# Kernel optimization log

Hardware: AMD Instinct MI355X
Metric: run time of the kernel (lower is better)

The kernel has to match this reference:

```python
import jax, jax.numpy as jnp
import numpy as np

QMAX = 127.0  # int8 symmetric range


def _fake_quant(x, axes):
    """AQT-style int8 symmetric fake-quant over contraction axes.

    Returns quantized integer values (stored as f32) and per-channel scales
    (keepdims over `axes`).
    """
    absmax = jnp.max(jnp.abs(x), axis=axes, keepdims=True)
    scale = jnp.where(absmax > 0, absmax / QMAX, jnp.ones_like(absmax))
    q = jnp.clip(jnp.round(x / scale), -QMAX, QMAX)
    return q, scale


def setup_inputs() -> dict:
    key = jax.random.key(0)
    k1, k2 = jax.random.split(key)
    lhs = jax.random.normal(k1, (4, 16384, 512), dtype=jnp.float32)
    rhs = jax.random.normal(k2, (512, 512), dtype=jnp.float32)
    return {"lhs": lhs, "rhs": rhs}


def reference(lhs, rhs):
    # dimension_numbers = (((2,), (0,)), ((), ())) -- Dense-style contraction.
    # Quantize each operand symmetrically to int8 along its contraction axis.
    lhs_q, lhs_scale = _fake_quant(lhs, axes=(2,))   # lhs_q: [B,S,D], scale: [B,S,1]
    rhs_q, rhs_scale = _fake_quant(rhs, axes=(0,))   # rhs_q: [D,F], scale: [1,F]
    # Integer-valued matmul (accumulation exact in f32 for these magnitudes),
    # then dequantize with the outer product of scales.
    acc = jnp.einsum('bsd,df->bsf', lhs_q, rhs_q)    # [B,S,F]
    return acc * lhs_scale * rhs_scale               # broadcast [B,S,1]*[1,F]
```

## Files before the change

kernel.cpp:

```cpp
#include <hip/hip_runtime.h>
#include <hip/hip_bf16.h>
#include <stdint.h>

#define QMAX 127.0f

typedef __attribute__((ext_vector_type(4))) int   i32x4;
typedef __attribute__((ext_vector_type(2))) int   i32x2;
typedef __attribute__((ext_vector_type(4))) float f32x4v;

typedef __attribute__((address_space(1))) const void GVoid;
typedef __attribute__((address_space(3))) void LVoid;

__device__ inline int quant_i(float x, float inv) {
    float q = rintf(x * inv);
    q = fminf(fmaxf(q, -QMAX), QMAX);
    return (int)q;
}

__device__ inline uint32_t pack4(f32x4v v, float inv) {
    return (uint32_t)(quant_i(v.x, inv) & 255)
         | ((uint32_t)(quant_i(v.y, inv) & 255) << 8)
         | ((uint32_t)(quant_i(v.z, inv) & 255) << 16)
         | ((uint32_t)(quant_i(v.w, inv) & 255) << 24);
}

__device__ inline float amax8(f32x4v a, f32x4v b) {
    return fmaxf(fmaxf(fmaxf(fabsf(a.x), fabsf(a.y)), fmaxf(fabsf(a.z), fabsf(a.w))),
                 fmaxf(fmaxf(fabsf(b.x), fabsf(b.y)), fmaxf(fabsf(b.z), fabsf(b.w))));
}

__global__ __launch_bounds__(256, 8) void quant_kernel(const float* __restrict__ lhs,
                                                       const float* __restrict__ rhs,
                                                       int8_t* __restrict__ Aq,
                                                       int8_t* __restrict__ Bt,
                                                       float* __restrict__ lscale,
                                                       float* __restrict__ rscale,
                                                       int nLhs) {
    const int lane = threadIdx.x & 63;
    const int wave = threadIdx.x >> 6;
    const int bid  = blockIdx.x;

    if (bid >= nLhs) {
        const int f = (bid - nLhs) * 4 + wave;
        float v[8];
        float amax = 0.f;
#pragma unroll
        for (int i = 0; i < 8; ++i) {
            v[i] = rhs[(size_t)(lane + 64 * i) * 512 + f];
            amax = fmaxf(amax, fabsf(v[i]));
        }
#pragma unroll
        for (int m = 1; m <= 32; m <<= 1)
            amax = fmaxf(amax, __shfl_xor(amax, m, 64));
        const float inv = amax > 0.f ? QMAX / amax : 0.f;
        if (lane == 0) rscale[f] = amax > 0.f ? amax * (1.0f / QMAX) : 1.0f;
#pragma unroll
        for (int i = 0; i < 8; ++i)
            Bt[(size_t)f * 512 + lane + 64 * i] = (int8_t)quant_i(v[i], inv);
        return;
    }

    const int row0 = bid * 32 + wave * 8;
    const float* rp = lhs + (size_t)row0 * 512 + lane * 8;
    int8_t* op = Aq + (size_t)row0 * 512 + lane * 8;
#pragma unroll
    for (int r = 0; r < 8; r += 2) {
        const f32x4v a0 = __builtin_nontemporal_load((const f32x4v*)(rp + (size_t)r * 512));
        const f32x4v b0 = __builtin_nontemporal_load((const f32x4v*)(rp + (size_t)r * 512 + 4));
        const f32x4v a1 = __builtin_nontemporal_load((const f32x4v*)(rp + (size_t)(r + 1) * 512));
        const f32x4v b1 = __builtin_nontemporal_load((const f32x4v*)(rp + (size_t)(r + 1) * 512 + 4));
        float m0 = amax8(a0, b0);
        float m1 = amax8(a1, b1);
#pragma unroll
        for (int m = 1; m <= 32; m <<= 1) {
            m0 = fmaxf(m0, __shfl_xor(m0, m, 64));
            m1 = fmaxf(m1, __shfl_xor(m1, m, 64));
        }
        const float inv0 = m0 > 0.f ? QMAX / m0 : 0.f;
        const float inv1 = m1 > 0.f ? QMAX / m1 : 0.f;
        if (lane == 0) {
            lscale[row0 + r]     = m0 > 0.f ? m0 * (1.0f / QMAX) : 1.0f;
            lscale[row0 + r + 1] = m1 > 0.f ? m1 * (1.0f / QMAX) : 1.0f;
        }
        i32x2 p0, p1;
        p0.x = (int)pack4(a0, inv0); p0.y = (int)pack4(b0, inv0);
        p1.x = (int)pack4(a1, inv1); p1.y = (int)pack4(b1, inv1);
        *(i32x2*)(op + (size_t)r * 512)       = p0;
        *(i32x2*)(op + (size_t)(r + 1) * 512) = p1;
    }
}

__global__ __launch_bounds__(256, 2) void gemm_kernel(const int8_t* __restrict__ Aq,
                                                      const int8_t* __restrict__ Bt,
                                                      const float* __restrict__ lscale,
                                                      const float* __restrict__ rscale,
                                                      float* __restrict__ out) {
    __shared__ int8_t lds[65536];

    const int tid  = threadIdx.x;
    const int lane = tid & 63;
    const int wave = tid >> 6;
    const int wr   = wave >> 1;
    const int wc   = wave & 1;

    const int g   = blockIdx.x;
    const int xcd = g & 7;
    const int j   = g >> 3;
    const int m0  = (xcd * 64 + (j >> 2)) * 128;
    const int n0  = (j & 3) * 128;

    const int lane15 = lane & 15;
    const int laneHi = lane >> 4;
    const int chunkBase = wave * 1024;

    i32x4 acc[4][4];
#pragma unroll
    for (int i = 0; i < 4; ++i)
#pragma unroll
        for (int jj = 0; jj < 4; ++jj)
            acc[i][jj] = (i32x4){0, 0, 0, 0};

#define STAGE(KT, BUF)                                                              \
    {                                                                               \
        _Pragma("unroll")                                                           \
        for (int c = 0; c < 4; ++c) {                                               \
            const int chunk = c * 4096 + chunkBase;                                 \
            const int d     = chunk + lane * 16;                                    \
            const int row   = d >> 7;                                               \
            const int srck  = (d & 127) ^ ((row & 7) << 4);                         \
            const int8_t* sA = Aq + (size_t)(m0 + row) * 512 + (KT) + srck;         \
            __builtin_amdgcn_global_load_lds((GVoid*)sA, (LVoid*)(lds + (BUF) + chunk), 16, 0, 0); \
            const int8_t* sB = Bt + (size_t)(n0 + row) * 512 + (KT) + srck;         \
            __builtin_amdgcn_global_load_lds((GVoid*)sB, (LVoid*)(lds + (BUF) + 16384 + chunk), 16, 0, 0); \
        }                                                                           \
    }

    STAGE(0, 0)
    __syncthreads();

#pragma unroll
    for (int t = 0; t < 4; ++t) {
        const int buf = (t & 1) * 32768;
        if (t < 3) STAGE((t + 1) * 128, (~t & 1) * 32768)

        i32x4 af[4][2], bf[4][2];
#pragma unroll
        for (int mi = 0; mi < 4; ++mi) {
            const int row = wr * 64 + mi * 16 + lane15;
            const int sw  = (row & 7) << 4;
#pragma unroll
            for (int kk = 0; kk < 2; ++kk) {
                const int kb = kk * 64 + laneHi * 16;
                af[mi][kk] = *(const i32x4*)(lds + buf + row * 128 + (kb ^ sw));
            }
        }
#pragma unroll
        for (int ni = 0; ni < 4; ++ni) {
            const int col = wc * 64 + ni * 16 + lane15;
            const int sw  = (col & 7) << 4;
#pragma unroll
            for (int kk = 0; kk < 2; ++kk) {
                const int kb = kk * 64 + laneHi * 16;
                bf[ni][kk] = *(const i32x4*)(lds + buf + 16384 + col * 128 + (kb ^ sw));
            }
        }
#pragma unroll
        for (int kk = 0; kk < 2; ++kk)
#pragma unroll
            for (int mi = 0; mi < 4; ++mi)
#pragma unroll
                for (int ni = 0; ni < 4; ++ni)
                    acc[mi][ni] = __builtin_amdgcn_mfma_i32_16x16x64_i8(
                        af[mi][kk], bf[ni][kk], acc[mi][ni], 0, 0, 0);

        if (t < 3) __syncthreads();
    }
#undef STAGE

    float rs[4];
#pragma unroll
    for (int ni = 0; ni < 4; ++ni)
        rs[ni] = rscale[n0 + wc * 64 + ni * 16 + lane15];
    const int rg = laneHi * 4;
#pragma unroll
    for (int mi = 0; mi < 4; ++mi) {
#pragma unroll
        for (int r = 0; r < 4; ++r) {
            const int grow = m0 + wr * 64 + mi * 16 + rg + r;
            const float ls = lscale[grow];
            float* op = out + (size_t)grow * 512 + n0 + wc * 64;
#pragma unroll
            for (int ni = 0; ni < 4; ++ni)
                __builtin_nontemporal_store(acc[mi][ni][r] * ls * rs[ni],
                                            op + ni * 16 + lane15);
        }
    }
}

extern "C" void kernel_launch(void* const* d_in, const int* in_sizes, int n_in,
                              void* d_out, int out_size, void* d_ws, size_t ws_size,
                              hipStream_t stream) {
    const float* lhs = (const float*)d_in[0];
    const float* rhs = (const float*)d_in[1];
    float* out = (float*)d_out;

    char* ws = (char*)d_ws;
    int8_t* Bt    = (int8_t*)ws;
    float* rscale = (float*)(ws + 262144);
    float* lscale = (float*)(ws + 266240);
    int8_t* Aq    = (int8_t*)(ws + 1048576);

    const int rows = in_sizes[0] / 512;
    const int nLhs = rows / 32;

    quant_kernel<<<nLhs + 128, 256, 0, stream>>>(lhs, rhs, Aq, Bt, lscale, rscale, nLhs);
    gemm_kernel<<<(rows / 128) * 4, 256, 0, stream>>>(Aq, Bt, lscale, rscale, out);
}
```

Baseline: 77.31 us.

## Drop GEMM LDS double buffering to single buffer for higher occupancy

The GEMM kernel now uses one 32 KB LDS buffer instead of a 64 KB double buffer. It raises the launch-bounds occupancy hint from 2 to 3 blocks per CU, so more blocks can hide load latency. Each k-tile now loads, syncs, computes and syncs again, which gives up the overlap of prefetching the next tile with MFMA work. The output stores also change from nontemporal to plain stores.

```diff
diff --git a/kernel.cpp b/kernel.cpp
--- a/kernel.cpp
+++ b/kernel.cpp
@@ -90,12 +90,12 @@
     }
 }
 
-__global__ __launch_bounds__(256, 2) void gemm_kernel(const int8_t* __restrict__ Aq,
+__global__ __launch_bounds__(256, 3) void gemm_kernel(const int8_t* __restrict__ Aq,
                                                       const int8_t* __restrict__ Bt,
                                                       const float* __restrict__ lscale,
                                                       const float* __restrict__ rscale,
                                                       float* __restrict__ out) {
-    __shared__ int8_t lds[65536];
+    __shared__ int8_t lds[32768];
 
     const int tid  = threadIdx.x;
     const int lane = tid & 63;
@@ -109,39 +109,32 @@
     const int m0  = (xcd * 64 + (j >> 2)) * 128;
     const int n0  = (j & 3) * 128;
 
+    i32x4 acc[4][4];
+#pragma unroll
+    for (int i = 0; i < 4; ++i)
+#pragma unroll
+        for (int jj = 0; jj < 4; ++jj)
+            acc[i][jj] = (i32x4){0, 0, 0, 0};
+
     const int lane15 = lane & 15;
     const int laneHi = lane >> 4;
-    const int chunkBase = wave * 1024;
-
-    i32x4 acc[4][4];
-#pragma unroll
-    for (int i = 0; i < 4; ++i)
-#pragma unroll
-        for (int jj = 0; jj < 4; ++jj)
-            acc[i][jj] = (i32x4){0, 0, 0, 0};
-
-#define STAGE(KT, BUF)                                                              \
-    {                                                                               \
-        _Pragma("unroll")                                                           \
-        for (int c = 0; c < 4; ++c) {                                               \
-            const int chunk = c * 4096 + chunkBase;                                 \
-            const int d     = chunk + lane * 16;                                    \
-            const int row   = d >> 7;                                               \
-            const int srck  = (d & 127) ^ ((row & 7) << 4);                         \
-            const int8_t* sA = Aq + (size_t)(m0 + row) * 512 + (KT) + srck;         \
-            __builtin_amdgcn_global_load_lds((GVoid*)sA, (LVoid*)(lds + (BUF) + chunk), 16, 0, 0); \
-            const int8_t* sB = Bt + (size_t)(n0 + row) * 512 + (KT) + srck;         \
-            __builtin_amdgcn_global_load_lds((GVoid*)sB, (LVoid*)(lds + (BUF) + 16384 + chunk), 16, 0, 0); \
-        }                                                                           \
-    }
-
-    STAGE(0, 0)
-    __syncthreads();
-
-#pragma unroll
-    for (int t = 0; t < 4; ++t) {
-        const int buf = (t & 1) * 32768;
-        if (t < 3) STAGE((t + 1) * 128, (~t & 1) * 32768)
+
+#pragma unroll
+    for (int kt = 0; kt < 512; kt += 128) {
+        __syncthreads();
+#pragma unroll
+        for (int c = 0; c < 4; ++c) {
+            const int chunk = (c * 4 + wave) * 1024;
+            const int d     = chunk + lane * 16;
+            const int row   = d >> 7;
+            const int koff  = d & 127;
+            const int srck  = koff ^ ((row & 7) << 4);
+            const int8_t* srcA = Aq + (size_t)(m0 + row) * 512 + kt + srck;
+            __builtin_amdgcn_global_load_lds((GVoid*)srcA, (LVoid*)(lds + chunk), 16, 0, 0);
+            const int8_t* srcB = Bt + (size_t)(n0 + row) * 512 + kt + srck;
+            __builtin_amdgcn_global_load_lds((GVoid*)srcB, (LVoid*)(lds + 16384 + chunk), 16, 0, 0);
+        }
+        __syncthreads();
 
         i32x4 af[4][2], bf[4][2];
 #pragma unroll
@@ -151,7 +144,7 @@
 #pragma unroll
             for (int kk = 0; kk < 2; ++kk) {
                 const int kb = kk * 64 + laneHi * 16;
-                af[mi][kk] = *(const i32x4*)(lds + buf + row * 128 + (kb ^ sw));
+                af[mi][kk] = *(const i32x4*)(lds + row * 128 + (kb ^ sw));
             }
         }
 #pragma unroll
@@ -161,7 +154,7 @@
 #pragma unroll
             for (int kk = 0; kk < 2; ++kk) {
                 const int kb = kk * 64 + laneHi * 16;
-                bf[ni][kk] = *(const i32x4*)(lds + buf + 16384 + col * 128 + (kb ^ sw));
+                bf[ni][kk] = *(const i32x4*)(lds + 16384 + col * 128 + (kb ^ sw));
             }
         }
 #pragma unroll
@@ -172,10 +165,7 @@
                 for (int ni = 0; ni < 4; ++ni)
                     acc[mi][ni] = __builtin_amdgcn_mfma_i32_16x16x64_i8(
                         af[mi][kk], bf[ni][kk], acc[mi][ni], 0, 0, 0);
-
-        if (t < 3) __syncthreads();
-    }
-#undef STAGE
+    }
 
     float rs[4];
 #pragma unroll
@@ -191,8 +181,7 @@
             float* op = out + (size_t)grow * 512 + n0 + wc * 64;
 #pragma unroll
             for (int ni = 0; ni < 4; ++ni)
-                __builtin_nontemporal_store(acc[mi][ni][r] * ls * rs[ni],
-                                            op + ni * 16 + lane15);
+                op[ni * 16 + lane15] = (float)acc[mi][ni][r] * ls * rs[ni];
         }
     }
 }
```

After: 70.95 us. 1.09x faster.
